# Kernel optimization log

Hardware: AMD Instinct MI355X
Metric: run time of the kernel (lower is better)

Reference implementation:

```python
import jax, jax.numpy as jnp
import numpy as np

B, ND, NE, D, H = 2, 2048, 2048, 1024, 16
HD = D // H
DFF = 4 * D
EPS = 1e-5


def setup_inputs() -> dict:
    key = jax.random.key(0)
    ks = jax.random.split(key, 16)
    s = lambda fan_in: 1.0 / np.sqrt(fan_in)
    inp = {
        'x': jax.random.normal(ks[0], (B, ND, D), jnp.float32),
        'memory': jax.random.normal(ks[1], (B, NE, D), jnp.float32),
        'ln1_g': jnp.ones((D,), jnp.float32), 'ln1_b': jnp.zeros((D,), jnp.float32),
        'Wqkv': jax.random.normal(ks[2], (D, 3 * D), jnp.float32) * s(D),
        'Wo_sa': jax.random.normal(ks[3], (D, D), jnp.float32) * s(D),
        'bo_sa': jnp.zeros((D,), jnp.float32),
        'ln2_g': jnp.ones((D,), jnp.float32), 'ln2_b': jnp.zeros((D,), jnp.float32),
        'Wq': jax.random.normal(ks[4], (D, D), jnp.float32) * s(D),
        'Wk': jax.random.normal(ks[5], (D, D), jnp.float32) * s(D),
        'Wv': jax.random.normal(ks[6], (D, D), jnp.float32) * s(D),
        'Wo_ca': jax.random.normal(ks[7], (D, D), jnp.float32) * s(D),
        'bo_ca': jnp.zeros((D,), jnp.float32),
        'ln3_g': jnp.ones((D,), jnp.float32), 'ln3_b': jnp.zeros((D,), jnp.float32),
        'W1': jax.random.normal(ks[8], (D, DFF), jnp.float32) * s(D),
        'b1': jnp.zeros((DFF,), jnp.float32),
        'W2': jax.random.normal(ks[9], (DFF, D), jnp.float32) * s(DFF),
        'b2': jnp.zeros((D,), jnp.float32),
        'attn_mask': jnp.tril(jnp.ones((ND, ND), jnp.bool_)),
    }
    return inp


def _layernorm(x, g, b):
    mu = jnp.mean(x, axis=-1, keepdims=True)
    var = jnp.mean(jnp.square(x - mu), axis=-1, keepdims=True)
    return (x - mu) * jax.lax.rsqrt(var + EPS) * g + b


def _heads(t, n):  # (B,N,D) -> (B,H,N,HD)
    Bn = t.shape[0]
    return t.reshape(Bn, n, H, HD).transpose(0, 2, 1, 3)


def _attend(q, k, v, mask=None):
    scale = HD ** -0.5
    scores = jnp.einsum('bhqd,bhkd->bhqk', q, k) * scale
    if mask is not None:
        scores = jnp.where(mask, scores, -jnp.inf)
    attn = jax.nn.softmax(scores, axis=-1)
    out = jnp.einsum('bhqk,bhkd->bhqd', attn, v)
    Bn, _, Nq, _ = out.shape
    return out.transpose(0, 2, 1, 3).reshape(Bn, Nq, D)


def reference(x, memory, ln1_g, ln1_b, Wqkv, Wo_sa, bo_sa, ln2_g, ln2_b,
              Wq, Wk, Wv, Wo_ca, bo_ca, ln3_g, ln3_b, W1, b1, W2, b2, attn_mask):
    # --- masked self-attention ---
    h = _layernorm(x, ln1_g, ln1_b)
    qkv = (h @ Wqkv).reshape(B, ND, 3, H, HD).transpose(2, 0, 3, 1, 4)  # (3,B,H,N,HD)
    q, k, v = qkv[0], qkv[1], qkv[2]
    sa = _attend(q, k, v, attn_mask[None, None]) @ Wo_sa + bo_sa
    x = x + sa
    # --- cross-attention ---
    h = _layernorm(x, ln2_g, ln2_b)
    q = _heads(h @ Wq, ND)
    k = _heads(memory @ Wk, NE)
    v = _heads(memory @ Wv, NE)
    ca = _attend(q, k, v) @ Wo_ca + bo_ca
    x = x + ca
    # --- FFN ---
    h = _layernorm(x, ln3_g, ln3_b)
    x = x + (jax.nn.gelu(h @ W1 + b1, approximate=False) @ W2 + b2)
    return x
```

## Files before the change

kernel.cpp:

```cpp
#include <hip/hip_runtime.h>
#include <hip/hip_bf16.h>
#include <math.h>

#define B_   2
#define ND_  2048
#define NE_  2048
#define D_   1024
#define H_   16
#define HD_  64
#define DFF_ 4096
#define T_   4096

typedef __attribute__((ext_vector_type(8))) short bf16x8;
typedef __attribute__((ext_vector_type(4))) float f32x4;

#if __has_builtin(__builtin_amdgcn_exp2f)
#define EXP2(x) __builtin_amdgcn_exp2f(x)
#else
#define EXP2(x) exp2f(x)
#endif

__device__ __forceinline__ short f2bf(float f) {
  union { float f; unsigned u; } v; v.f = f;
  return (short)((v.u + 0x7FFFu + ((v.u >> 16) & 1u)) >> 16);
}
__device__ __forceinline__ float bf2f(short s) {
  union { unsigned u; float f; } v; v.u = ((unsigned)(unsigned short)s) << 16;
  return v.f;
}

typedef const __attribute__((address_space(1))) void gvoid_t;
typedef __attribute__((address_space(3))) void lvoid_t;

__device__ __forceinline__ void gload16(const void* src, void* dst) {
  __builtin_amdgcn_global_load_lds((gvoid_t*)src, (lvoid_t*)dst, 16, 0, 0);
}

__global__ __launch_bounds__(256) void prep(
    const float* __restrict__ Wqkv, short* __restrict__ wqkv_t,
    const float* __restrict__ W1, short* __restrict__ w1_t,
    const float* __restrict__ W2, short* __restrict__ w2_t,
    const float* __restrict__ i0, const float* __restrict__ i1,
    const float* __restrict__ i2, const float* __restrict__ i3,
    const float* __restrict__ i4,
    short* __restrict__ o0, short* __restrict__ o1, short* __restrict__ o2,
    short* __restrict__ o3, short* __restrict__ o4,
    const float* __restrict__ mem, short* __restrict__ membf) {
  const int id = blockIdx.x;
  const int tid = threadIdx.x;
  if (id >= 16384) {
    const int i = (id - 16384) * 256 + tid;
    float4 v = ((const float4*)mem)[i];
    short4 o;
    o.x = f2bf(v.x); o.y = f2bf(v.y); o.z = f2bf(v.z); o.w = f2bf(v.w);
    ((short4*)membf)[i] = o;
    return;
  }
  const float* in; short* out; int K, N, bx, by;
  if (id < 3072) {
    in = Wqkv; out = wqkv_t; K = 1024; N = 3072; bx = id % 96; by = id / 96;
  } else if (id < 7168) {
    const int t = id - 3072;
    in = W1; out = w1_t; K = 1024; N = 4096; bx = t % 128; by = t / 128;
  } else if (id < 11264) {
    const int t = id - 7168;
    in = W2; out = w2_t; K = 4096; N = 1024; bx = t % 32; by = t / 32;
  } else {
    const int t = id - 11264;
    const int z = t >> 10, r = t & 1023;
    bx = r % 32; by = r / 32; K = 1024; N = 1024;
    in  = z == 0 ? i0 : z == 1 ? i1 : z == 2 ? i2 : z == 3 ? i3 : i4;
    out = z == 0 ? o0 : z == 1 ? o1 : z == 2 ? o2 : z == 3 ? o3 : o4;
  }
  __shared__ float tb[32][33];
  const int tx = tid & 31, ty = tid >> 5;
  const int n0 = bx * 32, k0 = by * 32;
#pragma unroll
  for (int i = 0; i < 4; ++i)
    tb[ty + i * 8][tx] = in[(size_t)(k0 + ty + i * 8) * N + n0 + tx];
  __syncthreads();
#pragma unroll
  for (int i = 0; i < 4; ++i)
    out[(size_t)(n0 + ty + i * 8) * K + k0 + tx] = f2bf(tb[tx][ty + i * 8]);
}

__global__ __launch_bounds__(256) void ln_kernel(const float* __restrict__ x,
                                                 const float* __restrict__ g,
                                                 const float* __restrict__ b,
                                                 short* __restrict__ out) {
  const int row = blockIdx.x;
  const int tid = threadIdx.x;
  const float* xr = x + (size_t)row * D_;
  float4 v = reinterpret_cast<const float4*>(xr)[tid];
  float s  = v.x + v.y + v.z + v.w;
  float s2 = v.x * v.x + v.y * v.y + v.z * v.z + v.w * v.w;
#pragma unroll
  for (int m = 1; m < 64; m <<= 1) {
    s  += __shfl_xor(s, m);
    s2 += __shfl_xor(s2, m);
  }
  __shared__ float ss[4], ss2[4];
  const int w = tid >> 6;
  if ((tid & 63) == 0) { ss[w] = s; ss2[w] = s2; }
  __syncthreads();
  s  = ss[0] + ss[1] + ss[2] + ss[3];
  s2 = ss2[0] + ss2[1] + ss2[2] + ss2[3];
  const float mu   = s * (1.0f / D_);
  const float var  = s2 * (1.0f / D_) - mu * mu;
  const float rstd = rsqrtf(var + 1e-5f);
  float4 gv = reinterpret_cast<const float4*>(g)[tid];
  float4 bv = reinterpret_cast<const float4*>(b)[tid];
  short4 o;
  o.x = f2bf((v.x - mu) * rstd * gv.x + bv.x);
  o.y = f2bf((v.y - mu) * rstd * gv.y + bv.y);
  o.z = f2bf((v.z - mu) * rstd * gv.z + bv.z);
  o.w = f2bf((v.w - mu) * rstd * gv.w + bv.w);
  reinterpret_cast<short4*>(out + (size_t)row * D_)[tid] = o;
}

__global__ __launch_bounds__(256) void ln_fused(const float* __restrict__ xprev,
                                                const short* delta,
                                                const float* __restrict__ pbias,
                                                const float* __restrict__ g,
                                                const float* __restrict__ b,
                                                short* out_ln,
                                                float* __restrict__ out_x) {
  const int row = blockIdx.x;
  const int tid = threadIdx.x;
  float4 v = reinterpret_cast<const float4*>(xprev + (size_t)row * D_)[tid];
  short4 dv = reinterpret_cast<const short4*>(delta + (size_t)row * D_)[tid];
  float4 pb = reinterpret_cast<const float4*>(pbias)[tid];
  v.x += bf2f(dv.x) + pb.x;
  v.y += bf2f(dv.y) + pb.y;
  v.z += bf2f(dv.z) + pb.z;
  v.w += bf2f(dv.w) + pb.w;
  float s  = v.x + v.y + v.z + v.w;
  float s2 = v.x * v.x + v.y * v.y + v.z * v.z + v.w * v.w;
#pragma unroll
  for (int m = 1; m < 64; m <<= 1) {
    s  += __shfl_xor(s, m);
    s2 += __shfl_xor(s2, m);
  }
  __shared__ float ss[4], ss2[4];
  const int w = tid >> 6;
  if ((tid & 63) == 0) { ss[w] = s; ss2[w] = s2; }
  __syncthreads();
  s  = ss[0] + ss[1] + ss[2] + ss[3];
  s2 = ss2[0] + ss2[1] + ss2[2] + ss2[3];
  const float mu   = s * (1.0f / D_);
  const float var  = s2 * (1.0f / D_) - mu * mu;
  const float rstd = rsqrtf(var + 1e-5f);
  reinterpret_cast<float4*>(out_x + (size_t)row * D_)[tid] = v;
  float4 gv = reinterpret_cast<const float4*>(g)[tid];
  float4 bv = reinterpret_cast<const float4*>(b)[tid];
  short4 o;
  o.x = f2bf((v.x - mu) * rstd * gv.x + bv.x);
  o.y = f2bf((v.y - mu) * rstd * gv.y + bv.y);
  o.z = f2bf((v.z - mu) * rstd * gv.z + bv.z);
  o.w = f2bf((v.w - mu) * rstd * gv.w + bv.w);
  reinterpret_cast<short4*>(out_ln + (size_t)row * D_)[tid] = o;
}

__global__ __launch_bounds__(256) void addbias(const float* __restrict__ x,
                                               const short* __restrict__ delta,
                                               const float* __restrict__ bias,
                                               float* __restrict__ out) {
  const int i = blockIdx.x * 256 + threadIdx.x;
  float4 v = ((const float4*)x)[i];
  short4 dv = ((const short4*)delta)[i];
  const int col = (i * 4) & (D_ - 1);
  float4 pb = *(const float4*)(bias + col);
  v.x += bf2f(dv.x) + pb.x;
  v.y += bf2f(dv.y) + pb.y;
  v.z += bf2f(dv.z) + pb.z;
  v.w += bf2f(dv.w) + pb.w;
  ((float4*)out)[i] = v;
}

template <int MODE>
__global__ __launch_bounds__(256) void gemm_bt(const short* __restrict__ A,
                                               const short* __restrict__ Bt,
                                               const float* __restrict__ bias,
                                               void* __restrict__ Cout,
                                               int M, int N, int K) {
  __shared__ short As[2][128 * 64];
  __shared__ short Bs[2][128 * 64];
  const int tid = threadIdx.x;
  const int gx = gridDim.x;
  const int nwg = gx * gridDim.y;
  int lin = blockIdx.y * gx + blockIdx.x;
  lin = (lin & 7) * (nwg >> 3) + (lin >> 3);
  const int m0 = (lin / gx) * 128, n0 = (lin % gx) * 128;
  const int wave = tid >> 6, lane = tid & 63;
  const int wm = (wave >> 1) * 64, wn = (wave & 1) * 64;
  const int lr = lane & 15, lg = lane >> 4;
  const int lx = lr & 7;

  f32x4 acc[4][4];
#pragma unroll
  for (int i = 0; i < 4; ++i)
#pragma unroll
    for (int j = 0; j < 4; ++j) acc[i][j] = f32x4{0.f, 0.f, 0.f, 0.f};

  const int sr = tid >> 3;
  const int scs = ((tid & 7) ^ (sr & 7)) * 8;
  const size_t arow = (size_t)(m0 + sr) * K + scs;
  const size_t brow = (size_t)(n0 + sr) * K + scs;

  auto stage = [&](int buf, int k0) {
#pragma unroll
    for (int p = 0; p < 4; ++p) {
      gload16(A + arow + (size_t)(p * 32) * K + k0, &As[buf][p * 2048 + tid * 8]);
      gload16(Bt + brow + (size_t)(p * 32) * K + k0, &Bs[buf][p * 2048 + tid * 8]);
    }
  };

  stage(0, 0);
  __syncthreads();
  int cur = 0;
  for (int k0 = 0; k0 < K; k0 += 64) {
    if (k0 + 64 < K) stage(cur ^ 1, k0 + 64);
    const short* Ab = &As[cur][0];
    const short* Bb = &Bs[cur][0];
#pragma unroll
    for (int kk = 0; kk < 2; ++kk) {
      bf16x8 af[4], bfr[4];
#pragma unroll
      for (int mi = 0; mi < 4; ++mi)
        af[mi] = *(const bf16x8*)(Ab + (wm + mi * 16 + lr) * 64 +
                                  (((kk * 4 + lg) ^ lx) * 8));
#pragma unroll
      for (int ni = 0; ni < 4; ++ni)
        bfr[ni] = *(const bf16x8*)(Bb + (wn + ni * 16 + lr) * 64 +
                                   (((kk * 4 + lg) ^ lx) * 8));
#pragma unroll
      for (int mi = 0; mi < 4; ++mi)
#pragma unroll
        for (int ni = 0; ni < 4; ++ni)
          acc[mi][ni] = __builtin_amdgcn_mfma_f32_16x16x32_bf16(
              af[mi], bfr[ni], acc[mi][ni], 0, 0, 0);
    }
    __syncthreads();
    cur ^= 1;
  }

#pragma unroll
  for (int mi = 0; mi < 4; ++mi) {
    const int row = m0 + wm + mi * 16 + lg * 4;
#pragma unroll
    for (int ni = 0; ni < 4; ++ni) {
      const int col = n0 + wn + ni * 16 + lr;
#pragma unroll
      for (int r = 0; r < 4; ++r) {
        const size_t idx = (size_t)(row + r) * N + col;
        const float v = acc[mi][ni][r];
        if (MODE == 0) {
          ((short*)Cout)[idx] = f2bf(v);
        } else {
          const float tt = v + bias[col];
          const float yy = fmaf(tt * tt * tt, 0.044715f, tt);
          const float e = EXP2(yy * -2.3022343813918633f);
          ((short*)Cout)[idx] = f2bf(tt / (1.0f + e));
        }
      }
    }
  }
}

__global__ __launch_bounds__(256) void gemm_bt3(const short* __restrict__ A0,
                                                const short* __restrict__ A1,
                                                const short* __restrict__ A2,
                                                const short* __restrict__ B0,
                                                const short* __restrict__ B1,
                                                const short* __restrict__ B2,
                                                short* __restrict__ C0,
                                                short* __restrict__ C1,
                                                short* __restrict__ C2,
                                                int M, int N, int K) {
  const int z = blockIdx.z;
  const short* A  = z == 0 ? A0 : (z == 1 ? A1 : A2);
  const short* Bt = z == 0 ? B0 : (z == 1 ? B1 : B2);
  short* C        = z == 0 ? C0 : (z == 1 ? C1 : C2);

  __shared__ short As[2][128 * 64];
  __shared__ short Bs[2][128 * 64];
  const int tid = threadIdx.x;
  const int gx = gridDim.x;
  const int nwg = gx * gridDim.y;
  int lin = blockIdx.y * gx + blockIdx.x;
  lin = (lin & 7) * (nwg >> 3) + (lin >> 3);
  const int m0 = (lin / gx) * 128, n0 = (lin % gx) * 128;
  const int wave = tid >> 6, lane = tid & 63;
  const int wm = (wave >> 1) * 64, wn = (wave & 1) * 64;
  const int lr = lane & 15, lg = lane >> 4;
  const int lx = lr & 7;

  f32x4 acc[4][4];
#pragma unroll
  for (int i = 0; i < 4; ++i)
#pragma unroll
    for (int j = 0; j < 4; ++j) acc[i][j] = f32x4{0.f, 0.f, 0.f, 0.f};

  const int sr = tid >> 3;
  const int scs = ((tid & 7) ^ (sr & 7)) * 8;
  const size_t arow = (size_t)(m0 + sr) * K + scs;
  const size_t brow = (size_t)(n0 + sr) * K + scs;

  auto stage = [&](int buf, int k0) {
#pragma unroll
    for (int p = 0; p < 4; ++p) {
      gload16(A + arow + (size_t)(p * 32) * K + k0, &As[buf][p * 2048 + tid * 8]);
      gload16(Bt + brow + (size_t)(p * 32) * K + k0, &Bs[buf][p * 2048 + tid * 8]);
    }
  };

  stage(0, 0);
  __syncthreads();
  int cur = 0;
  for (int k0 = 0; k0 < K; k0 += 64) {
    if (k0 + 64 < K) stage(cur ^ 1, k0 + 64);
    const short* Ab = &As[cur][0];
    const short* Bb = &Bs[cur][0];
#pragma unroll
    for (int kk = 0; kk < 2; ++kk) {
      bf16x8 af[4], bfr[4];
#pragma unroll
      for (int mi = 0; mi < 4; ++mi)
        af[mi] = *(const bf16x8*)(Ab + (wm + mi * 16 + lr) * 64 +
                                  (((kk * 4 + lg) ^ lx) * 8));
#pragma unroll
      for (int ni = 0; ni < 4; ++ni)
        bfr[ni] = *(const bf16x8*)(Bb + (wn + ni * 16 + lr) * 64 +
                                   (((kk * 4 + lg) ^ lx) * 8));
#pragma unroll
      for (int mi = 0; mi < 4; ++mi)
#pragma unroll
        for (int ni = 0; ni < 4; ++ni)
          acc[mi][ni] = __builtin_amdgcn_mfma_f32_16x16x32_bf16(
              af[mi], bfr[ni], acc[mi][ni], 0, 0, 0);
    }
    __syncthreads();
    cur ^= 1;
  }

#pragma unroll
  for (int mi = 0; mi < 4; ++mi) {
    const int row = m0 + wm + mi * 16 + lg * 4;
#pragma unroll
    for (int ni = 0; ni < 4; ++ni) {
      const int col = n0 + wn + ni * 16 + lr;
#pragma unroll
      for (int r = 0; r < 4; ++r)
        C[(size_t)(row + r) * N + col] = f2bf(acc[mi][ni][r]);
    }
  }
}

__global__ __launch_bounds__(256) void gemm_bt64(const short* __restrict__ A,
                                                 const short* __restrict__ Bt,
                                                 short* __restrict__ Cout,
                                                 int M, int N, int K) {
  __shared__ short As[2][64 * 64];
  __shared__ short Bs[2][128 * 64];
  const int tid = threadIdx.x;
  const int gx = gridDim.x;
  const int nwg = gx * gridDim.y;
  int lin = blockIdx.y * gx + blockIdx.x;
  lin = (lin & 7) * (nwg >> 3) + (lin >> 3);
  const int m0 = (lin / gx) * 64, n0 = (lin % gx) * 128;
  const int wave = tid >> 6, lane = tid & 63;
  const int wn = wave * 32;
  const int lr = lane & 15, lg = lane >> 4;
  const int lx = lr & 7;

  f32x4 acc[4][2];
#pragma unroll
  for (int i = 0; i < 4; ++i)
#pragma unroll
    for (int j = 0; j < 2; ++j) acc[i][j] = f32x4{0.f, 0.f, 0.f, 0.f};

  const int sr = tid >> 3;
  const int scs = ((tid & 7) ^ (sr & 7)) * 8;
  const size_t arow = (size_t)(m0 + sr) * K + scs;
  const size_t brow = (size_t)(n0 + sr) * K + scs;

  auto stage = [&](int buf, int k0) {
#pragma unroll
    for (int p = 0; p < 2; ++p)
      gload16(A + arow + (size_t)(p * 32) * K + k0, &As[buf][p * 2048 + tid * 8]);
#pragma unroll
    for (int p = 0; p < 4; ++p)
      gload16(Bt + brow + (size_t)(p * 32) * K + k0, &Bs[buf][p * 2048 + tid * 8]);
  };

  stage(0, 0);
  __syncthreads();
  int cur = 0;
  for (int k0 = 0; k0 < K; k0 += 64) {
    if (k0 + 64 < K) stage(cur ^ 1, k0 + 64);
    const short* Ab = &As[cur][0];
    const short* Bb = &Bs[cur][0];
#pragma unroll
    for (int kk = 0; kk < 2; ++kk) {
      bf16x8 af[4], bfr[2];
#pragma unroll
      for (int mi = 0; mi < 4; ++mi)
        af[mi] = *(const bf16x8*)(Ab + (mi * 16 + lr) * 64 +
                                  (((kk * 4 + lg) ^ lx) * 8));
#pragma unroll
      for (int ni = 0; ni < 2; ++ni)
        bfr[ni] = *(const bf16x8*)(Bb + (wn + ni * 16 + lr) * 64 +
                                   (((kk * 4 + lg) ^ lx) * 8));
#pragma unroll
      for (int mi = 0; mi < 4; ++mi)
#pragma unroll
        for (int ni = 0; ni < 2; ++ni)
          acc[mi][ni] = __builtin_amdgcn_mfma_f32_16x16x32_bf16(
              af[mi], bfr[ni], acc[mi][ni], 0, 0, 0);
    }
    __syncthreads();
    cur ^= 1;
  }

#pragma unroll
  for (int mi = 0; mi < 4; ++mi) {
    const int row = m0 + mi * 16 + lg * 4;
#pragma unroll
    for (int ni = 0; ni < 2; ++ni) {
      const int col = n0 + wn + ni * 16 + lr;
#pragma unroll
      for (int r = 0; r < 4; ++r)
        Cout[(size_t)(row + r) * N + col] = f2bf(acc[mi][ni][r]);
    }
  }
}

__global__ __launch_bounds__(256) void vtrans(const short* __restrict__ in,
                                              short* __restrict__ out,
                                              int ldi, int N) {
  const int bh = blockIdx.z;
  const int b = bh >> 4, h = bh & 15;
  const short* ib = in + (size_t)b * N * ldi + h * HD_;
  short* ob = out + (size_t)bh * HD_ * N;
  __shared__ short t[32][33];
  const int tx = threadIdx.x, ty = threadIdx.y;
  const int n0 = blockIdx.x * 32, d0 = blockIdx.y * 32;
#pragma unroll
  for (int i = 0; i < 4; ++i)
    t[ty + i * 8][tx] = ib[(size_t)(n0 + ty + i * 8) * ldi + d0 + tx];
  __syncthreads();
#pragma unroll
  for (int i = 0; i < 4; ++i)
    ob[(size_t)(d0 + ty + i * 8) * N + n0 + tx] = t[tx][ty + i * 8];
}

__global__ __launch_bounds__(512) void flash(const short* __restrict__ Q,
                                             const short* __restrict__ Kp,
                                             const short* __restrict__ Vt,
                                             short* __restrict__ O,
                                             int ldq, int ldk, int ldo,
                                             int NK, int causal) {
  const int bh = blockIdx.x;
  int qb = blockIdx.y;
  if (causal) qb = (qb < 8) ? (2 * qb) : (31 - 2 * qb);
  const int b = bh >> 4, h = bh & 15;
  const int q0 = qb * 128;
  const int tid = threadIdx.x, wave = tid >> 6, lane = tid & 63;
  const int lr = lane & 15, lg = lane >> 4;
  const int lx = lr & 7;

  const short* Qb = Q + (size_t)b * ND_ * ldq + h * HD_;
  const short* Kb = Kp + (size_t)b * NK * ldk + h * HD_;
  const short* Vb = Vt + (size_t)bh * HD_ * NK;
  short* Ob = O + (size_t)b * ND_ * ldo + h * HD_;

  __shared__ short Ks[2][64 * 64];
  __shared__ short Vs[2][64 * 64];
  __shared__ short Ps[8][16 * 64];

  const int qrow = q0 + wave * 16 + lr;
  const bf16x8 qf0 = *(const bf16x8*)(Qb + (size_t)qrow * ldq + lg * 8);
  const bf16x8 qf1 = *(const bf16x8*)(Qb + (size_t)qrow * ldq + 32 + lg * 8);

  const bf16x8 ONES = {0x3F80, 0x3F80, 0x3F80, 0x3F80,
                       0x3F80, 0x3F80, 0x3F80, 0x3F80};

  f32x4 oacc[4];
  f32x4 lacc = f32x4{0.f, 0.f, 0.f, 0.f};
  float m_own = -1e30f;
#pragma unroll
  for (int i = 0; i < 4; ++i) oacc[i] = f32x4{0.f, 0.f, 0.f, 0.f};

  const int sr0 = tid >> 3;
  const int ssw = ((tid & 7) ^ (sr0 & 7)) * 8;
  const int e0 = tid * 8;

  const float SC = 0.18033688011112042f;

  short* Pw = &Ps[wave][0];
  const int pbase = lr * 64 + (lg & 1) * 4;

  auto stage = [&](int buf, int k0) {
    gload16(Kb + (size_t)(k0 + sr0) * ldk + ssw, &Ks[buf][0] + e0);
    gload16(Vb + (size_t)sr0 * NK + k0 + ssw, &Vs[buf][0] + e0);
  };

  const int nkt = causal ? (2 * qb + 2) : (NK / 64);
  stage(0, 0);
  __syncthreads();
  int cur = 0;
  for (int t = 0; t < nkt; ++t) {
    const int k0 = t * 64;
    if (t + 1 < nkt) stage(cur ^ 1, k0 + 64);
    if (!causal || k0 <= q0 + wave * 16 + 15) {
      const short* Ksb = &Ks[cur][0];
      const short* Vsb = &Vs[cur][0];

      f32x4 st[4];
#pragma unroll
      for (int kb = 0; kb < 4; ++kb) {
        const bf16x8 kf0 = *(const bf16x8*)(Ksb + (kb * 16 + lr) * 64 + ((lg ^ lx) * 8));
        const bf16x8 kf1 = *(const bf16x8*)(Ksb + (kb * 16 + lr) * 64 + (((4 + lg) ^ lx) * 8));
        st[kb] = f32x4{0.f, 0.f, 0.f, 0.f};
        st[kb] = __builtin_amdgcn_mfma_f32_16x16x32_bf16(kf0, qf0, st[kb], 0, 0, 0);
        st[kb] = __builtin_amdgcn_mfma_f32_16x16x32_bf16(kf1, qf1, st[kb], 0, 0, 0);
      }
      if (causal && k0 + 63 > q0 + wave * 16) {
#pragma unroll
        for (int kb = 0; kb < 4; ++kb)
#pragma unroll
          for (int r = 0; r < 4; ++r)
            if ((k0 + kb * 16 + lg * 4 + r) > qrow) st[kb][r] = -3.0e38f;
      }

      float rm = st[0][0];
#pragma unroll
      for (int kb = 0; kb < 4; ++kb)
#pragma unroll
        for (int r = 0; r < 4; ++r)
          if (kb || r) rm = fmaxf(rm, st[kb][r]);
      rm = fmaxf(rm, __shfl_xor(rm, 16));
      rm = fmaxf(rm, __shfl_xor(rm, 32));

      if (!__all(rm - m_own <= 44.f)) {
        const float nm = fmaxf(m_own, rm);
        const float fac = EXP2((m_own - nm) * SC);
        m_own = nm;
        const float fr0 = __shfl(fac, (lg << 2) + 0);
        const float fr1 = __shfl(fac, (lg << 2) + 1);
        const float fr2 = __shfl(fac, (lg << 2) + 2);
        const float fr3 = __shfl(fac, (lg << 2) + 3);
#pragma unroll
        for (int db = 0; db < 4; ++db) {
          oacc[db][0] *= fr0; oacc[db][1] *= fr1;
          oacc[db][2] *= fr2; oacc[db][3] *= fr3;
        }
        lacc[0] *= fr0; lacc[1] *= fr1; lacc[2] *= fr2; lacc[3] *= fr3;
      }
      const float nmsc = m_own * SC;
#pragma unroll
      for (int kb = 0; kb < 4; ++kb)
#pragma unroll
        for (int r = 0; r < 4; ++r)
          st[kb][r] = EXP2(fmaf(st[kb][r], SC, -nmsc));

#pragma unroll
      for (int kb = 0; kb < 4; ++kb) {
        union { unsigned u[2]; unsigned long long ull; } pk;
        asm("v_cvt_pk_bf16_f32 %0, %1, %2"
            : "=v"(pk.u[0]) : "v"(st[kb][0]), "v"(st[kb][1]));
        asm("v_cvt_pk_bf16_f32 %0, %1, %2"
            : "=v"(pk.u[1]) : "v"(st[kb][2]), "v"(st[kb][3]));
        const int cs = kb * 2 + (lg >> 1);
        *(unsigned long long*)(Pw + pbase + ((cs ^ lx) * 8)) = pk.ull;
      }
      const bf16x8 pf0 = *(const bf16x8*)(Pw + lr * 64 + ((lg ^ lx) * 8));
      const bf16x8 pf1 = *(const bf16x8*)(Pw + lr * 64 + (((4 + lg) ^ lx) * 8));

#pragma unroll
      for (int db = 0; db < 4; ++db) {
        const bf16x8 vf0 = *(const bf16x8*)(Vsb + (db * 16 + lr) * 64 + ((lg ^ lx) * 8));
        const bf16x8 vf1 = *(const bf16x8*)(Vsb + (db * 16 + lr) * 64 + (((4 + lg) ^ lx) * 8));
        oacc[db] = __builtin_amdgcn_mfma_f32_16x16x32_bf16(pf0, vf0, oacc[db], 0, 0, 0);
        oacc[db] = __builtin_amdgcn_mfma_f32_16x16x32_bf16(pf1, vf1, oacc[db], 0, 0, 0);
      }
      lacc = __builtin_amdgcn_mfma_f32_16x16x32_bf16(pf0, ONES, lacc, 0, 0, 0);
      lacc = __builtin_amdgcn_mfma_f32_16x16x32_bf16(pf1, ONES, lacc, 0, 0, 0);
    }
    __syncthreads();
    cur ^= 1;
  }
#pragma unroll
  for (int db = 0; db < 4; ++db)
#pragma unroll
    for (int r = 0; r < 4; ++r) {
      const int q = q0 + wave * 16 + lg * 4 + r;
      Ob[(size_t)q * ldo + db * 16 + lr] = f2bf(oacc[db][r] / lacc[r]);
    }
}

extern "C" void kernel_launch(void* const* d_in, const int* in_sizes, int n_in,
                              void* d_out, int out_size, void* d_ws, size_t ws_size,
                              hipStream_t stream) {
  const float* x      = (const float*)d_in[0];
  const float* memory = (const float*)d_in[1];
  const float* ln1_g  = (const float*)d_in[2];
  const float* ln1_b  = (const float*)d_in[3];
  const float* Wqkv   = (const float*)d_in[4];
  const float* Wo_sa  = (const float*)d_in[5];
  const float* bo_sa  = (const float*)d_in[6];
  const float* ln2_g  = (const float*)d_in[7];
  const float* ln2_b  = (const float*)d_in[8];
  const float* Wq     = (const float*)d_in[9];
  const float* Wk     = (const float*)d_in[10];
  const float* Wv     = (const float*)d_in[11];
  const float* Wo_ca  = (const float*)d_in[12];
  const float* bo_ca  = (const float*)d_in[13];
  const float* ln3_g  = (const float*)d_in[14];
  const float* ln3_b  = (const float*)d_in[15];
  const float* W1     = (const float*)d_in[16];
  const float* b1     = (const float*)d_in[17];
  const float* W2     = (const float*)d_in[18];
  const float* b2     = (const float*)d_in[19];

  char* ws = (char*)d_ws;
  size_t o = 0;
  auto alloc = [&](size_t bytes) { char* p = ws + o; o += bytes; return p; };
  short* wqkv_t = (short*)alloc((size_t)3072 * 1024 * 2);
  short* wosa_t = (short*)alloc((size_t)1024 * 1024 * 2);
  short* wq_t   = (short*)alloc((size_t)1024 * 1024 * 2);
  short* wk_t   = (short*)alloc((size_t)1024 * 1024 * 2);
  short* wv_t   = (short*)alloc((size_t)1024 * 1024 * 2);
  short* woca_t = (short*)alloc((size_t)1024 * 1024 * 2);
  short* w1_t   = (short*)alloc((size_t)4096 * 1024 * 2);
  short* w2_t   = (short*)alloc((size_t)1024 * 4096 * 2);
  short* hbf    = (short*)alloc((size_t)T_ * 1024 * 2);
  short* bufa   = (short*)alloc((size_t)T_ * 3072 * 2);
  short* vt     = (short*)alloc((size_t)32 * 64 * 2048 * 2);
  short* attn   = (short*)alloc((size_t)T_ * 1024 * 2);
  short* membf  = (short*)alloc((size_t)T_ * 1024 * 2);
  float* x1     = (float*)alloc((size_t)T_ * 1024 * 4);
  float* x2     = (float*)alloc((size_t)T_ * 1024 * 4);
  if (o > ws_size) return;

  short* ffn = bufa;
  short* qca = bufa;
  short* kca = bufa + (size_t)T_ * 1024;
  short* vca = bufa + (size_t)2 * T_ * 1024;

  const dim3 tb(32, 8);

  prep<<<dim3(20480), 256, 0, stream>>>(Wqkv, wqkv_t, W1, w1_t, W2, w2_t,
                                        Wo_sa, Wq, Wk, Wv, Wo_ca,
                                        wosa_t, wq_t, wk_t, wv_t, woca_t,
                                        memory, membf);

  ln_kernel<<<dim3(T_), 256, 0, stream>>>(x, ln1_g, ln1_b, hbf);
  gemm_bt<0><<<dim3(3072 / 128, T_ / 128), 256, 0, stream>>>(
      hbf, wqkv_t, nullptr, bufa, T_, 3072, 1024);
  vtrans<<<dim3(ND_ / 32, HD_ / 32, 32), tb, 0, stream>>>(bufa + 2048, vt, 3072, ND_);
  flash<<<dim3(32, ND_ / 128), 512, 0, stream>>>(
      bufa, bufa + 1024, vt, attn, 3072, 3072, 1024, ND_, 1);
  gemm_bt64<<<dim3(1024 / 128, T_ / 64), 256, 0, stream>>>(
      attn, wosa_t, hbf, T_, 1024, 1024);
  ln_fused<<<dim3(T_), 256, 0, stream>>>(x, hbf, bo_sa, ln2_g, ln2_b, hbf, x1);

  gemm_bt3<<<dim3(1024 / 128, T_ / 128, 3), 256, 0, stream>>>(
      hbf, membf, membf, wq_t, wk_t, wv_t, qca, kca, vca, T_, 1024, 1024);
  vtrans<<<dim3(NE_ / 32, HD_ / 32, 32), tb, 0, stream>>>(vca, vt, 1024, NE_);
  flash<<<dim3(32, ND_ / 128), 512, 0, stream>>>(
      qca, kca, vt, attn, 1024, 1024, 1024, NE_, 0);
  gemm_bt64<<<dim3(1024 / 128, T_ / 64), 256, 0, stream>>>(
      attn, woca_t, hbf, T_, 1024, 1024);
  ln_fused<<<dim3(T_), 256, 0, stream>>>(x1, hbf, bo_ca, ln3_g, ln3_b, hbf, x2);

  gemm_bt<2><<<dim3(4096 / 128, T_ / 128), 256, 0, stream>>>(
      hbf, w1_t, b1, ffn, T_, 4096, 1024);
  gemm_bt64<<<dim3(1024 / 128, T_ / 64), 256, 0, stream>>>(
      ffn, w2_t, hbf, T_, 1024, 4096);
  addbias<<<dim3((T_ * 1024) / (256 * 4)), 256, 0, stream>>>(
      x2, hbf, b2, (float*)d_out);
}
```

Measured before the change: 367.5 us.

## Split-K the N=1024 GEMMs in two and sum partials in epilogue kernels

The output-projection and FFN-down GEMMs now run with a z-dimension of two, each block computing half of K and writing a separate bf16 partial into a reused scratch buffer. The following layernorm and residual/bias kernels read both partials and add them. This doubles the block count to improve CU occupancy for the narrow N=1024 GEMMs, at the cost of extra partial-result memory traffic and an extra bf16 rounding of each partial.

```diff
diff --git a/kernel.cpp b/kernel.cpp
--- a/kernel.cpp
+++ b/kernel.cpp
@@ -118,22 +118,24 @@
   reinterpret_cast<short4*>(out + (size_t)row * D_)[tid] = o;
 }
 
-__global__ __launch_bounds__(256) void ln_fused(const float* __restrict__ xprev,
-                                                const short* delta,
-                                                const float* __restrict__ pbias,
-                                                const float* __restrict__ g,
-                                                const float* __restrict__ b,
-                                                short* out_ln,
-                                                float* __restrict__ out_x) {
+__global__ __launch_bounds__(256) void ln_fused2(const float* __restrict__ xprev,
+                                                 const short* d1,
+                                                 const short* __restrict__ d2,
+                                                 const float* __restrict__ pbias,
+                                                 const float* __restrict__ g,
+                                                 const float* __restrict__ b,
+                                                 short* out_ln,
+                                                 float* __restrict__ out_x) {
   const int row = blockIdx.x;
   const int tid = threadIdx.x;
   float4 v = reinterpret_cast<const float4*>(xprev + (size_t)row * D_)[tid];
-  short4 dv = reinterpret_cast<const short4*>(delta + (size_t)row * D_)[tid];
+  short4 dv = reinterpret_cast<const short4*>(d1 + (size_t)row * D_)[tid];
+  short4 d2v = reinterpret_cast<const short4*>(d2 + (size_t)row * D_)[tid];
   float4 pb = reinterpret_cast<const float4*>(pbias)[tid];
-  v.x += bf2f(dv.x) + pb.x;
-  v.y += bf2f(dv.y) + pb.y;
-  v.z += bf2f(dv.z) + pb.z;
-  v.w += bf2f(dv.w) + pb.w;
+  v.x += bf2f(dv.x) + bf2f(d2v.x) + pb.x;
+  v.y += bf2f(dv.y) + bf2f(d2v.y) + pb.y;
+  v.z += bf2f(dv.z) + bf2f(d2v.z) + pb.z;
+  v.w += bf2f(dv.w) + bf2f(d2v.w) + pb.w;
   float s  = v.x + v.y + v.z + v.w;
   float s2 = v.x * v.x + v.y * v.y + v.z * v.z + v.w * v.w;
 #pragma unroll
@@ -161,19 +163,21 @@
   reinterpret_cast<short4*>(out_ln + (size_t)row * D_)[tid] = o;
 }
 
-__global__ __launch_bounds__(256) void addbias(const float* __restrict__ x,
-                                               const short* __restrict__ delta,
-                                               const float* __restrict__ bias,
-                                               float* __restrict__ out) {
+__global__ __launch_bounds__(256) void addbias2(const float* __restrict__ x,
+                                                const short* __restrict__ d1,
+                                                const short* __restrict__ d2,
+                                                const float* __restrict__ bias,
+                                                float* __restrict__ out) {
   const int i = blockIdx.x * 256 + threadIdx.x;
   float4 v = ((const float4*)x)[i];
-  short4 dv = ((const short4*)delta)[i];
+  short4 dv = ((const short4*)d1)[i];
+  short4 d2v = ((const short4*)d2)[i];
   const int col = (i * 4) & (D_ - 1);
   float4 pb = *(const float4*)(bias + col);
-  v.x += bf2f(dv.x) + pb.x;
-  v.y += bf2f(dv.y) + pb.y;
-  v.z += bf2f(dv.z) + pb.z;
-  v.w += bf2f(dv.w) + pb.w;
+  v.x += bf2f(dv.x) + bf2f(d2v.x) + pb.x;
+  v.y += bf2f(dv.y) + bf2f(d2v.y) + pb.y;
+  v.z += bf2f(dv.z) + bf2f(d2v.z) + pb.z;
+  v.w += bf2f(dv.w) + bf2f(d2v.w) + pb.w;
   ((float4*)out)[i] = v;
 }
 
@@ -356,13 +360,18 @@
   }
 }
 
-__global__ __launch_bounds__(256) void gemm_bt64(const short* __restrict__ A,
-                                                 const short* __restrict__ Bt,
-                                                 short* __restrict__ Cout,
-                                                 int M, int N, int K) {
+__global__ __launch_bounds__(256) void gemm_bt64_sk(const short* __restrict__ A,
+                                                    const short* __restrict__ Bt,
+                                                    short* __restrict__ C0,
+                                                    short* __restrict__ C1,
+                                                    int M, int N, int K) {
   __shared__ short As[2][64 * 64];
   __shared__ short Bs[2][128 * 64];
   const int tid = threadIdx.x;
+  const int z = blockIdx.z;
+  const int Kh = K >> 1;
+  const int kbase = z * Kh;
+  short* Cout = z ? C1 : C0;
   const int gx = gridDim.x;
   const int nwg = gx * gridDim.y;
   int lin = blockIdx.y * gx + blockIdx.x;
@@ -381,8 +390,8 @@
 
   const int sr = tid >> 3;
   const int scs = ((tid & 7) ^ (sr & 7)) * 8;
-  const size_t arow = (size_t)(m0 + sr) * K + scs;
-  const size_t brow = (size_t)(n0 + sr) * K + scs;
+  const size_t arow = (size_t)(m0 + sr) * K + kbase + scs;
+  const size_t brow = (size_t)(n0 + sr) * K + kbase + scs;
 
   auto stage = [&](int buf, int k0) {
 #pragma unroll
@@ -396,8 +405,8 @@
   stage(0, 0);
   __syncthreads();
   int cur = 0;
-  for (int k0 = 0; k0 < K; k0 += 64) {
-    if (k0 + 64 < K) stage(cur ^ 1, k0 + 64);
+  for (int k0 = 0; k0 < Kh; k0 += 64) {
+    if (k0 + 64 < Kh) stage(cur ^ 1, k0 + 64);
     const short* Ab = &As[cur][0];
     const short* Bb = &Bs[cur][0];
 #pragma unroll
@@ -661,23 +670,23 @@
   vtrans<<<dim3(ND_ / 32, HD_ / 32, 32), tb, 0, stream>>>(bufa + 2048, vt, 3072, ND_);
   flash<<<dim3(32, ND_ / 128), 512, 0, stream>>>(
       bufa, bufa + 1024, vt, attn, 3072, 3072, 1024, ND_, 1);
-  gemm_bt64<<<dim3(1024 / 128, T_ / 64), 256, 0, stream>>>(
-      attn, wosa_t, hbf, T_, 1024, 1024);
-  ln_fused<<<dim3(T_), 256, 0, stream>>>(x, hbf, bo_sa, ln2_g, ln2_b, hbf, x1);
+  gemm_bt64_sk<<<dim3(1024 / 128, T_ / 64, 2), 256, 0, stream>>>(
+      attn, wosa_t, hbf, vt, T_, 1024, 1024);
+  ln_fused2<<<dim3(T_), 256, 0, stream>>>(x, hbf, vt, bo_sa, ln2_g, ln2_b, hbf, x1);
 
   gemm_bt3<<<dim3(1024 / 128, T_ / 128, 3), 256, 0, stream>>>(
       hbf, membf, membf, wq_t, wk_t, wv_t, qca, kca, vca, T_, 1024, 1024);
   vtrans<<<dim3(NE_ / 32, HD_ / 32, 32), tb, 0, stream>>>(vca, vt, 1024, NE_);
   flash<<<dim3(32, ND_ / 128), 512, 0, stream>>>(
       qca, kca, vt, attn, 1024, 1024, 1024, NE_, 0);
-  gemm_bt64<<<dim3(1024 / 128, T_ / 64), 256, 0, stream>>>(
-      attn, woca_t, hbf, T_, 1024, 1024);
-  ln_fused<<<dim3(T_), 256, 0, stream>>>(x1, hbf, bo_ca, ln3_g, ln3_b, hbf, x2);
+  gemm_bt64_sk<<<dim3(1024 / 128, T_ / 64, 2), 256, 0, stream>>>(
+      attn, woca_t, hbf, vt, T_, 1024, 1024);
+  ln_fused2<<<dim3(T_), 256, 0, stream>>>(x1, hbf, vt, bo_ca, ln3_g, ln3_b, hbf, x2);
 
   gemm_bt<2><<<dim3(4096 / 128, T_ / 128), 256, 0, stream>>>(
       hbf, w1_t, b1, ffn, T_, 4096, 1024);
-  gemm_bt64<<<dim3(1024 / 128, T_ / 64), 256, 0, stream>>>(
-      ffn, w2_t, hbf, T_, 1024, 4096);
-  addbias<<<dim3((T_ * 1024) / (256 * 4)), 256, 0, stream>>>(
-      x2, hbf, b2, (float*)d_out);
-}
+  gemm_bt64_sk<<<dim3(1024 / 128, T_ / 64, 2), 256, 0, stream>>>(
+      ffn, w2_t, hbf, attn, T_, 1024, 4096);
+  addbias2<<<dim3((T_ * 1024) / (256 * 4)), 256, 0, stream>>>(
+      x2, hbf, attn, b2, (float*)d_out);
+}
```

After: 381.7 us. +3.9%, slower.

## Split cross-attention keys across two blocks and merge partial softmax results

Applied to the files above, without the earlier changes.

Replaces the single-pass cross-attention flash kernel with a split-K variant that launches twice as many blocks, each processing half of the memory keys and writing unnormalized bf16 partial outputs plus per-row max and sum. A merge kernel then combines the two halves with log-sum-exp rescaling. The aim is more parallelism (1024 blocks instead of 512) so the 256-CU GPU is better filled. The cost is an extra launch, extra memory traffic for partial outputs, and extra bf16 rounding of the unnormalized partials. Free hbf and membf buffers are reused to hold the partials.

```diff
diff --git a/kernel.cpp b/kernel.cpp
--- a/kernel.cpp
+++ b/kernel.cpp
@@ -597,6 +597,192 @@
       const int q = q0 + wave * 16 + lg * 4 + r;
       Ob[(size_t)q * ldo + db * 16 + lr] = f2bf(oacc[db][r] / lacc[r]);
     }
+}
+
+__global__ __launch_bounds__(512) void flash_sp(const short* __restrict__ Q,
+                                                const short* __restrict__ Kp,
+                                                const short* __restrict__ Vt,
+                                                short* __restrict__ O0,
+                                                short* __restrict__ O1,
+                                                float* __restrict__ ml,
+                                                int ldq, int ldk, int NK) {
+  const int bh = blockIdx.x;
+  const int qb = blockIdx.y;
+  const int z = blockIdx.z;
+  const int kbase = z * (NK >> 1);
+  const int b = bh >> 4, h = bh & 15;
+  const int q0 = qb * 128;
+  const int tid = threadIdx.x, wave = tid >> 6, lane = tid & 63;
+  const int lr = lane & 15, lg = lane >> 4;
+  const int lx = lr & 7;
+
+  const short* Qb = Q + (size_t)b * ND_ * ldq + h * HD_;
+  const short* Kb = Kp + (size_t)b * NK * ldk + h * HD_;
+  const short* Vb = Vt + (size_t)bh * HD_ * NK;
+  short* Ob = (z ? O1 : O0) + (size_t)b * ND_ * D_ + h * HD_;
+
+  __shared__ short Ks[2][64 * 64];
+  __shared__ short Vs[2][64 * 64];
+  __shared__ short Ps[8][16 * 64];
+
+  const int qrow = q0 + wave * 16 + lr;
+  const bf16x8 qf0 = *(const bf16x8*)(Qb + (size_t)qrow * ldq + lg * 8);
+  const bf16x8 qf1 = *(const bf16x8*)(Qb + (size_t)qrow * ldq + 32 + lg * 8);
+
+  const bf16x8 ONES = {0x3F80, 0x3F80, 0x3F80, 0x3F80,
+                       0x3F80, 0x3F80, 0x3F80, 0x3F80};
+
+  f32x4 oacc[4];
+  f32x4 lacc = f32x4{0.f, 0.f, 0.f, 0.f};
+  float m_own = -1e30f;
+#pragma unroll
+  for (int i = 0; i < 4; ++i) oacc[i] = f32x4{0.f, 0.f, 0.f, 0.f};
+
+  const int sr0 = tid >> 3;
+  const int ssw = ((tid & 7) ^ (sr0 & 7)) * 8;
+  const int e0 = tid * 8;
+
+  const float SC = 0.18033688011112042f;
+
+  short* Pw = &Ps[wave][0];
+  const int pbase = lr * 64 + (lg & 1) * 4;
+
+  auto stage = [&](int buf, int k0) {
+    gload16(Kb + (size_t)(kbase + k0 + sr0) * ldk + ssw, &Ks[buf][0] + e0);
+    gload16(Vb + (size_t)sr0 * NK + kbase + k0 + ssw, &Vs[buf][0] + e0);
+  };
+
+  const int nkt = NK >> 7;
+  stage(0, 0);
+  __syncthreads();
+  int cur = 0;
+  for (int t = 0; t < nkt; ++t) {
+    const int k0 = t * 64;
+    if (t + 1 < nkt) stage(cur ^ 1, k0 + 64);
+    {
+      const short* Ksb = &Ks[cur][0];
+      const short* Vsb = &Vs[cur][0];
+
+      f32x4 st[4];
+#pragma unroll
+      for (int kb = 0; kb < 4; ++kb) {
+        const bf16x8 kf0 = *(const bf16x8*)(Ksb + (kb * 16 + lr) * 64 + ((lg ^ lx) * 8));
+        const bf16x8 kf1 = *(const bf16x8*)(Ksb + (kb * 16 + lr) * 64 + (((4 + lg) ^ lx) * 8));
+        st[kb] = f32x4{0.f, 0.f, 0.f, 0.f};
+        st[kb] = __builtin_amdgcn_mfma_f32_16x16x32_bf16(kf0, qf0, st[kb], 0, 0, 0);
+        st[kb] = __builtin_amdgcn_mfma_f32_16x16x32_bf16(kf1, qf1, st[kb], 0, 0, 0);
+      }
+
+      float rm = st[0][0];
+#pragma unroll
+      for (int kb = 0; kb < 4; ++kb)
+#pragma unroll
+        for (int r = 0; r < 4; ++r)
+          if (kb || r) rm = fmaxf(rm, st[kb][r]);
+      rm = fmaxf(rm, __shfl_xor(rm, 16));
+      rm = fmaxf(rm, __shfl_xor(rm, 32));
+
+      if (!__all(rm - m_own <= 44.f)) {
+        const float nm = fmaxf(m_own, rm);
+        const float fac = EXP2((m_own - nm) * SC);
+        m_own = nm;
+        const float fr0 = __shfl(fac, (lg << 2) + 0);
+        const float fr1 = __shfl(fac, (lg << 2) + 1);
+        const float fr2 = __shfl(fac, (lg << 2) + 2);
+        const float fr3 = __shfl(fac, (lg << 2) + 3);
+#pragma unroll
+        for (int db = 0; db < 4; ++db) {
+          oacc[db][0] *= fr0; oacc[db][1] *= fr1;
+          oacc[db][2] *= fr2; oacc[db][3] *= fr3;
+        }
+        lacc[0] *= fr0; lacc[1] *= fr1; lacc[2] *= fr2; lacc[3] *= fr3;
+      }
+      const float nmsc = m_own * SC;
+#pragma unroll
+      for (int kb = 0; kb < 4; ++kb)
+#pragma unroll
+        for (int r = 0; r < 4; ++r)
+          st[kb][r] = EXP2(fmaf(st[kb][r], SC, -nmsc));
+
+#pragma unroll
+      for (int kb = 0; kb < 4; ++kb) {
+        union { unsigned u[2]; unsigned long long ull; } pk;
+        asm("v_cvt_pk_bf16_f32 %0, %1, %2"
+            : "=v"(pk.u[0]) : "v"(st[kb][0]), "v"(st[kb][1]));
+        asm("v_cvt_pk_bf16_f32 %0, %1, %2"
+            : "=v"(pk.u[1]) : "v"(st[kb][2]), "v"(st[kb][3]));
+        const int cs = kb * 2 + (lg >> 1);
+        *(unsigned long long*)(Pw + pbase + ((cs ^ lx) * 8)) = pk.ull;
+      }
+      const bf16x8 pf0 = *(const bf16x8*)(Pw + lr * 64 + ((lg ^ lx) * 8));
+      const bf16x8 pf1 = *(const bf16x8*)(Pw + lr * 64 + (((4 + lg) ^ lx) * 8));
+
+#pragma unroll
+      for (int db = 0; db < 4; ++db) {
+        const bf16x8 vf0 = *(const bf16x8*)(Vsb + (db * 16 + lr) * 64 + ((lg ^ lx) * 8));
+        const bf16x8 vf1 = *(const bf16x8*)(Vsb + (db * 16 + lr) * 64 + (((4 + lg) ^ lx) * 8));
+        oacc[db] = __builtin_amdgcn_mfma_f32_16x16x32_bf16(pf0, vf0, oacc[db], 0, 0, 0);
+        oacc[db] = __builtin_amdgcn_mfma_f32_16x16x32_bf16(pf1, vf1, oacc[db], 0, 0, 0);
+      }
+      lacc = __builtin_amdgcn_mfma_f32_16x16x32_bf16(pf0, ONES, lacc, 0, 0, 0);
+      lacc = __builtin_amdgcn_mfma_f32_16x16x32_bf16(pf1, ONES, lacc, 0, 0, 0);
+    }
+    __syncthreads();
+    cur ^= 1;
+  }
+#pragma unroll
+  for (int db = 0; db < 4; ++db)
+#pragma unroll
+    for (int r = 0; r < 4; ++r) {
+      const int q = q0 + wave * 16 + lg * 4 + r;
+      Ob[(size_t)q * D_ + db * 16 + lr] = f2bf(oacc[db][r]);
+    }
+  if (lg == 0) {
+    const int tq = b * ND_ + qrow;
+    ml[(size_t)z * 65536 + tq * 16 + h] = m_own;
+  }
+  if (lr == 0) {
+#pragma unroll
+    for (int r = 0; r < 4; ++r) {
+      const int tq = b * ND_ + q0 + wave * 16 + lg * 4 + r;
+      ml[131072 + (size_t)z * 65536 + tq * 16 + h] = lacc[r];
+    }
+  }
+}
+
+__global__ __launch_bounds__(256) void flash_merge(const short* __restrict__ O0,
+                                                   const short* __restrict__ O1,
+                                                   const float* __restrict__ ml,
+                                                   short* __restrict__ out) {
+  const float SC = 0.18033688011112042f;
+  const int gid = blockIdx.x * 256 + threadIdx.x;
+  const int t = gid >> 7;
+  const int c = gid & 127;
+  const int h = c >> 3;
+  const int d0 = (c & 7) * 8;
+  const int mlidx = t * 16 + h;
+  const float m1 = ml[mlidx],          l1 = ml[131072 + mlidx];
+  const float m2 = ml[65536 + mlidx],  l2 = ml[131072 + 65536 + mlidx];
+  const float M = fmaxf(m1, m2);
+  const float w1 = EXP2((m1 - M) * SC);
+  const float w2 = EXP2((m2 - M) * SC);
+  const float inv = 1.0f / (l1 * w1 + l2 * w2);
+  const size_t ob = (size_t)t * D_ + h * HD_ + d0;
+  short4 a0 = *(const short4*)(O0 + ob);
+  short4 a1 = *(const short4*)(O0 + ob + 4);
+  short4 b0 = *(const short4*)(O1 + ob);
+  short4 b1 = *(const short4*)(O1 + ob + 4);
+  short4 r0, r1;
+  r0.x = f2bf((bf2f(a0.x) * w1 + bf2f(b0.x) * w2) * inv);
+  r0.y = f2bf((bf2f(a0.y) * w1 + bf2f(b0.y) * w2) * inv);
+  r0.z = f2bf((bf2f(a0.z) * w1 + bf2f(b0.z) * w2) * inv);
+  r0.w = f2bf((bf2f(a0.w) * w1 + bf2f(b0.w) * w2) * inv);
+  r1.x = f2bf((bf2f(a1.x) * w1 + bf2f(b1.x) * w2) * inv);
+  r1.y = f2bf((bf2f(a1.y) * w1 + bf2f(b1.y) * w2) * inv);
+  r1.z = f2bf((bf2f(a1.z) * w1 + bf2f(b1.z) * w2) * inv);
+  r1.w = f2bf((bf2f(a1.w) * w1 + bf2f(b1.w) * w2) * inv);
+  *(short4*)(out + ob) = r0;
+  *(short4*)(out + ob + 4) = r1;
 }
 
 extern "C" void kernel_launch(void* const* d_in, const int* in_sizes, int n_in,
@@ -641,6 +827,7 @@
   short* membf  = (short*)alloc((size_t)T_ * 1024 * 2);
   float* x1     = (float*)alloc((size_t)T_ * 1024 * 4);
   float* x2     = (float*)alloc((size_t)T_ * 1024 * 4);
+  float* mlbuf  = (float*)alloc((size_t)4 * 65536 * 4);
   if (o > ws_size) return;
 
   short* ffn = bufa;
@@ -668,8 +855,10 @@
   gemm_bt3<<<dim3(1024 / 128, T_ / 128, 3), 256, 0, stream>>>(
       hbf, membf, membf, wq_t, wk_t, wv_t, qca, kca, vca, T_, 1024, 1024);
   vtrans<<<dim3(NE_ / 32, HD_ / 32, 32), tb, 0, stream>>>(vca, vt, 1024, NE_);
-  flash<<<dim3(32, ND_ / 128), 512, 0, stream>>>(
-      qca, kca, vt, attn, 1024, 1024, 1024, NE_, 0);
+  flash_sp<<<dim3(32, ND_ / 128, 2), 512, 0, stream>>>(
+      qca, kca, vt, hbf, membf, mlbuf, 1024, 1024, NE_);
+  flash_merge<<<dim3((T_ * 1024) / (256 * 8)), 256, 0, stream>>>(
+      hbf, membf, mlbuf, attn);
   gemm_bt64<<<dim3(1024 / 128, T_ / 64), 256, 0, stream>>>(
       attn, woca_t, hbf, T_, 1024, 1024);
   ln_fused<<<dim3(T_), 256, 0, stream>>>(x1, hbf, bo_ca, ln3_g, ln3_b, hbf, x2);
```

Result: no change. 374.2 us (+1.8%).
